# Kernel tuning notes

Measured on AMD Instinct MI355X. Metric: run time of the kernel, lower is better.

## Reference

```python
import jax, jax.numpy as jnp
import numpy as np

N = 100000          # num nodes
E = 1600000         # num edges (before self-loops)
IN = 128            # in_channels
HID = 32            # hidden_channels (= per-head dim, concat=False)
HEADS = 4
NEG_SLOPE = 0.2     # PyG GATConv default


def _glorot(k, shape):
    fan = shape[0] + shape[-1]
    return jax.random.normal(k, shape, jnp.float32) * np.float32(np.sqrt(2.0 / fan))


def setup_inputs() -> dict:
    key = jax.random.key(0)
    ks = jax.random.split(key, 18)
    inp = {}
    inp['x'] = jax.random.normal(ks[0], (N, IN), jnp.float32)
    inp['edge_index'] = jax.random.randint(ks[1], (2, E), 0, N, dtype=jnp.int64)
    dims_in = [IN, HID, HID]
    for i in range(3):
        inp[f'W{i+1}'] = _glorot(ks[2 + 4 * i], (dims_in[i], HEADS * HID))
        inp[f'as{i+1}'] = _glorot(ks[3 + 4 * i], (HEADS, HID))
        inp[f'ad{i+1}'] = _glorot(ks[4 + 4 * i], (HEADS, HID))
        inp[f'b{i+1}'] = jnp.zeros((HID,), jnp.float32)
    inp['lw1'] = _glorot(ks[14], (HID, HID // 2))
    inp['lb1'] = jnp.zeros((HID // 2,), jnp.float32)
    inp['lw2'] = _glorot(ks[15], (HID // 2, 1))
    inp['lb2'] = jnp.zeros((1,), jnp.float32)
    return inp


def gat_conv(x, src, dst, W, a_s, a_d, b):
    # x: [N, F_in]; src/dst: [E'] (self-loops included); concat=False -> head mean
    n = x.shape[0]
    h = (x @ W).reshape(n, HEADS, HID)                      # [N, H, C]
    alpha_src = jnp.einsum('nhc,hc->nh', h, a_s)            # [N, H]
    alpha_dst = jnp.einsum('nhc,hc->nh', h, a_d)            # [N, H]
    e = jax.nn.leaky_relu(alpha_src[src] + alpha_dst[dst], NEG_SLOPE)  # [E', H]
    # softmax over edges grouped by destination node
    e_max = jax.ops.segment_max(e, dst, num_segments=n)     # [N, H]
    e = jnp.exp(e - e_max[dst])
    denom = jax.ops.segment_sum(e, dst, num_segments=n)     # [N, H]
    alpha = e / (denom[dst] + 1e-16)                        # [E', H]
    msg = h[src] * alpha[:, :, None]                        # [E', H, C]
    out = jax.ops.segment_sum(msg, dst, num_segments=n)     # [N, H, C]
    return out.mean(axis=1) + b                             # concat=False: mean heads


def reference(x, edge_index, W1, as1, ad1, b1, W2, as2, ad2, b2, W3, as3, ad3, b3, lw1, lb1, lw2, lb2):
    # add self-loops (PyG GATConv default add_self_loops=True)
    loop = jnp.arange(N, dtype=edge_index.dtype)
    src = jnp.concatenate([edge_index[0], loop])
    dst = jnp.concatenate([edge_index[1], loop])
    h = jax.nn.relu(gat_conv(x, src, dst, W1, as1, ad1, b1))
    h = jax.nn.relu(gat_conv(h, src, dst, W2, as2, ad2, b2))
    h = jax.nn.relu(gat_conv(h, src, dst, W3, as3, ad3, b3))
    g = h.mean(axis=0, keepdims=True)                       # global_mean_pool, batch=None -> [1, HID]
    g = jax.nn.relu(g @ lw1 + lb1)                          # dropout is identity in eval
    return g @ lw2 + lb2                                    # [1, 1]
```

## Files before the change

### kernel.cpp

```cpp
#include <hip/hip_runtime.h>
#include <hip/hip_bf16.h>


#define HEADS 4
#define HID 32
#define F_HID 128
#define NEG_SLOPE 0.2f
#define BSHIFT 5
#define MAXB 3328

typedef float v2f __attribute__((ext_vector_type(2)));
using s8bf  = __attribute__((ext_vector_type(8))) short;
using f32x4 = __attribute__((ext_vector_type(4))) float;

__device__ __forceinline__ float lrelu(float v) { return v > 0.f ? v : NEG_SLOPE * v; }

__device__ __forceinline__ uint32_t bf16_rne(float f) {
    union { float f; uint32_t u; } c; c.f = f;
    return (c.u + 0x7fffu + ((c.u >> 16) & 1u)) >> 16;
}
__device__ __forceinline__ v2f up2(uint32_t u) {
    v2f r;
    r.x = __uint_as_float(u << 16);
    r.y = __uint_as_float(u & 0xffff0000u);
    return r;
}
__device__ __forceinline__ float bperm_f(int addr, float v) {
    return __int_as_float(__builtin_amdgcn_ds_bpermute(addr, __float_as_int(v)));
}
__device__ __forceinline__ int bperm_i(int addr, int v) {
    return __builtin_amdgcn_ds_bpermute(addr, v);
}
__device__ __forceinline__ v2f vshflxor(v2f v, int m) {
    v2f r; r.x = __shfl_xor(v.x, m); r.y = __shfl_xor(v.y, m); return r;
}


__global__ void deg_hist(const int* __restrict__ ei, int E, int* __restrict__ deg) {
    int i = blockIdx.x * blockDim.x + threadIdx.x;
    if (i < E) {
        int d = ei[E + i];
        atomicAdd(&deg[d], 1);
    }
}

__global__ void scan_partial(const int* __restrict__ deg, int n, int* __restrict__ partial) {
    __shared__ int sm[256];
    int t = threadIdx.x;
    int i = blockIdx.x * 256 + t;
    sm[t] = (i < n) ? deg[i] : 0;
    __syncthreads();
    for (int s = 128; s > 0; s >>= 1) {
        if (t < s) sm[t] += sm[t + s];
        __syncthreads();
    }
    if (t == 0) partial[blockIdx.x] = sm[0];
}

__global__ __launch_bounds__(512) void scan_exclusive(int* partial, int B) {
    __shared__ int sm[512];
    int t = threadIdx.x;
    int carry = 0;
    for (int base = 0; base < B; base += 512) {
        int v = (base + t < B) ? partial[base + t] : 0;
        sm[t] = v;
        __syncthreads();
        for (int s = 1; s < 512; s <<= 1) {
            int add = (t >= s) ? sm[t - s] : 0;
            __syncthreads();
            sm[t] += add;
            __syncthreads();
        }
        if (base + t < B) partial[base + t] = carry + sm[t] - v;
        carry += sm[511];
        __syncthreads();
    }
}

__global__ void scan_final(const int* __restrict__ deg, int n, const int* __restrict__ partial,
                           int* __restrict__ row_start, int* __restrict__ gcursor) {
    __shared__ int sm[256];
    int t = threadIdx.x;
    int i = blockIdx.x * 256 + t;
    int v = (i < n) ? deg[i] : 0;
    sm[t] = v;
    __syncthreads();
    for (int s = 1; s < 256; s <<= 1) {
        int add = (t >= s) ? sm[t - s] : 0;
        __syncthreads();
        sm[t] += add;
        __syncthreads();
    }
    if (i < n) {
        int excl = partial[blockIdx.x] + sm[t] - v;
        row_start[i] = excl;
        if ((i & 31) == 0) gcursor[i >> BSHIFT] = excl;
    }
}

__global__ __launch_bounds__(512) void bucket_scatter(const int* __restrict__ ei, int E, int nb,
                                                      int* __restrict__ gcursor,
                                                      uint32_t* __restrict__ tmp) {
    __shared__ int hist[MAXB];
    __shared__ int base[MAXB];
    int t = threadIdx.x;
    int per = (E + gridDim.x - 1) / gridDim.x;
    int e0 = blockIdx.x * per;
    int e1 = e0 + per; if (e1 > E) e1 = E;

    for (int i = t; i < nb; i += 512) hist[i] = 0;
    __syncthreads();
    for (int i = e0 + t; i < e1; i += 512) {
        int d = ei[E + i];
        atomicAdd(&hist[d >> BSHIFT], 1);
    }
    __syncthreads();
    for (int i = t; i < nb; i += 512) {
        int c = hist[i];
        base[i] = c ? atomicAdd(&gcursor[i], c) : 0;
        hist[i] = 0;
    }
    __syncthreads();
    for (int i = e0 + t; i < e1; i += 512) {
        int d = ei[E + i];
        int s = ei[i];
        int b = d >> BSHIFT;
        int loc = atomicAdd(&hist[b], 1);
        tmp[base[b] + loc] = ((uint32_t)s << BSHIFT) | (uint32_t)(d & 31);
    }
}

__global__ __launch_bounds__(256) void bucket_sort(const uint32_t* __restrict__ tmp,
                                                   const int* __restrict__ row_start,
                                                   int n, int E,
                                                   int* __restrict__ csr) {
    __shared__ int cur[32];
    int b = blockIdx.x;
    int node0 = b << BSHIFT;
    int base = row_start[node0];
    int node1 = node0 + 32;
    int end = (node1 < n) ? row_start[node1] : E;
    int cnt = end - base;
    int t = threadIdx.x;
    if (t < 32) {
        int nd = node0 + t;
        cur[t] = (nd < n) ? (row_start[nd] - base) : 0;
    }
    __syncthreads();
    for (int i = t; i < cnt; i += 256) {
        uint32_t v = tmp[base + i];
        int pos = atomicAdd(&cur[v & 31], 1);
        csr[base + pos] = (int)(v >> BSHIFT);
    }
}


template <int FIN>
__global__ void prep_w(const float* __restrict__ W, const float* __restrict__ a_s,
                       const float* __restrict__ a_d, unsigned short* __restrict__ wbt) {
    constexpr int LDK = FIN + 8;
    int t = blockIdx.x * 256 + threadIdx.x;
    if (t >= 144 * LDK) return;
    int r = t / LDK, k = t % LDK;
    float v = 0.f;
    if (k < FIN) {
        if (r < 128) {
            v = W[(size_t)k * F_HID + r];
        } else if (r < 136) {
            int j = r - 128;
            const float* av = (j < 4) ? a_s : a_d;
            int hd = j & 3;
            float s = 0.f;
            for (int c = 0; c < 32; c++)
                s += W[(size_t)k * F_HID + hd * 32 + c] * av[hd * 32 + c];
            v = s;
        }
    }
    wbt[t] = (unsigned short)bf16_rne(v);
}

template <int FIN>
__global__ __launch_bounds__(256) void gemm_mfma(const float* __restrict__ x,
                                                 const unsigned short* __restrict__ wbt,
                                                 uint32_t* __restrict__ hb,
                                                 float* __restrict__ asrc,
                                                 float* __restrict__ adst, int n) {
    constexpr int LDK = FIN + 8;
    __shared__ unsigned short wl[144 * LDK];
    __shared__ unsigned short xs[32 * LDK];
    int t = threadIdx.x;
    int base = blockIdx.x * 32;

    {
        const uint4* wg4 = (const uint4*)wbt;
        uint4* wl4 = (uint4*)wl;
        constexpr int W4 = 144 * LDK / 8;
        for (int i = t; i < W4; i += 256) wl4[i] = wg4[i];
    }
    {
        constexpr int XIT = 32 * FIN / 4;
        for (int idx = t; idx < XIT; idx += 256) {
            int node = idx / (FIN / 4);
            int k4 = (idx % (FIN / 4)) * 4;
            int gnode = base + node;
            float4 v;
            if (gnode < n) v = *(const float4*)&x[(size_t)gnode * FIN + k4];
            else { v.x = 0.f; v.y = 0.f; v.z = 0.f; v.w = 0.f; }
            unsigned short* dst = &xs[node * LDK + k4];
            dst[0] = (unsigned short)bf16_rne(v.x);
            dst[1] = (unsigned short)bf16_rne(v.y);
            dst[2] = (unsigned short)bf16_rne(v.z);
            dst[3] = (unsigned short)bf16_rne(v.w);
        }
    }
    __syncthreads();

    int w = t >> 6;
    int l = t & 63;
    int nt = w >> 1;
    int ct0 = (w & 1) ? 5 : 0;
    int ct1 = (w & 1) ? 9 : 5;
    int lr = l & 15, lg = l >> 4;
    int node = base + nt * 16 + lr;
    const unsigned short* xrow = &xs[(nt * 16 + lr) * LDK + lg * 8];

    for (int ct = ct0; ct < ct1; ct++) {
        f32x4 acc = {0.f, 0.f, 0.f, 0.f};
        const unsigned short* arow = &wl[(ct * 16 + lr) * LDK + lg * 8];
#pragma unroll
        for (int kt = 0; kt < FIN / 32; kt++) {
            s8bf a = *(const s8bf*)(arow + kt * 32);
            s8bf b = *(const s8bf*)(xrow + kt * 32);
            acc = __builtin_amdgcn_mfma_f32_16x16x32_bf16(a, b, acc, 0, 0, 0);
        }
        if (node < n) {
            if (ct < 8) {
                uint2 pp;
                pp.x = bf16_rne(acc[0]) | (bf16_rne(acc[1]) << 16);
                pp.y = bf16_rne(acc[2]) | (bf16_rne(acc[3]) << 16);
                *(uint2*)&hb[(size_t)node * 64 + ct * 8 + lg * 2] = pp;
            } else {
                float4 o; o.x = acc[0]; o.y = acc[1]; o.z = acc[2]; o.w = acc[3];
                if (lg == 0)      *(float4*)&asrc[node * 4] = o;
                else if (lg == 1) *(float4*)&adst[node * 4] = o;
            }
        }
    }
}

__global__ __launch_bounds__(256) void aggregate(const uint32_t* __restrict__ hb,
                                                 const float* __restrict__ asrc,
                                                 const float* __restrict__ adst,
                                                 const int* __restrict__ row_start,
                                                 const int* __restrict__ deg,
                                                 const int* __restrict__ csr_src,
                                                 const float* __restrict__ bias,
                                                 float* __restrict__ xout, int n) {
    int d = blockIdx.x * 4 + (threadIdx.x >> 6);
    if (d >= n) return;
    int l = threadIdx.x & 63;
    int hd = l >> 4;
    int ci = l & 15;
    int hh = (l & 15) >> 2;
    int permH = hh << 6;
    int permb = permH + (l >> 4) * 4;
    int rowoff = hh * 64 + (l & 3) * 16;

    int start = row_start[d];
    int cnt = deg[d];
    float ad = adst[d * HEADS + hd];
    float e_self = lrelu(asrc[d * HEADS + hd] + ad);
    const char* hbbase = (const char*)hb;

    uint4 us = *(const uint4*)(hbbase + (((uint32_t)d) << 8) + rowoff);

    float dsum = 0.f;
    v2f a0 = {0.f, 0.f}, a1 = {0.f, 0.f}, a2 = {0.f, 0.f}, a3 = {0.f, 0.f};
    const int* csr = csr_src + start;

#define ACC4(U, PJ)                         \
    {                                       \
        v2f p2 = {PJ, PJ};                  \
        a0 += p2 * up2((U).x);              \
        a1 += p2 * up2((U).y);              \
        a2 += p2 * up2((U).z);              \
        a3 += p2 * up2((U).w);              \
    }

    for (int j0 = 0; j0 < cnt; j0 += 32) {
        int ncnt = cnt - j0; if (ncnt > 32) ncnt = 32;
        int jA = j0 + ci;      if (jA > cnt - 1) jA = cnt - 1;
        int jB = j0 + 16 + ci; if (jB > cnt - 1) jB = cnt - 1;
        int s0 = csr[jA];
        int s1 = csr[jB];

        int sj0 = bperm_i(permb,      s0);
        int sj1 = bperm_i(permb + 16, s0);
        int sj2 = bperm_i(permb + 32, s0);
        int sj3 = bperm_i(permb + 48, s0);
        int sj4 = bperm_i(permb,      s1);
        int sj5 = bperm_i(permb + 16, s1);
        int sj6 = bperm_i(permb + 32, s1);
        int sj7 = bperm_i(permb + 48, s1);
        uint4 u0 = *(const uint4*)(hbbase + (((uint32_t)sj0) << 8) + rowoff);
        uint4 u1 = *(const uint4*)(hbbase + (((uint32_t)sj1) << 8) + rowoff);
        uint4 u2 = *(const uint4*)(hbbase + (((uint32_t)sj2) << 8) + rowoff);
        uint4 u3 = *(const uint4*)(hbbase + (((uint32_t)sj3) << 8) + rowoff);
        uint4 u4 = *(const uint4*)(hbbase + (((uint32_t)sj4) << 8) + rowoff);
        uint4 u5 = *(const uint4*)(hbbase + (((uint32_t)sj5) << 8) + rowoff);
        uint4 u6 = *(const uint4*)(hbbase + (((uint32_t)sj6) << 8) + rowoff);
        uint4 u7 = *(const uint4*)(hbbase + (((uint32_t)sj7) << 8) + rowoff);

        float pe0 = (ci < ncnt)      ? __expf(lrelu(asrc[s0 * HEADS + hd] + ad)) : 0.f;
        float pe1 = (ci + 16 < ncnt) ? __expf(lrelu(asrc[s1 * HEADS + hd] + ad)) : 0.f;
        dsum += pe0 + pe1;
        float pj0 = bperm_f(permb,      pe0);
        float pj1 = bperm_f(permb + 16, pe0);
        float pj2 = bperm_f(permb + 32, pe0);
        float pj3 = bperm_f(permb + 48, pe0);
        float pj4 = bperm_f(permb,      pe1);
        float pj5 = bperm_f(permb + 16, pe1);
        float pj6 = bperm_f(permb + 32, pe1);
        float pj7 = bperm_f(permb + 48, pe1);

        ACC4(u0, pj0); ACC4(u1, pj1); ACC4(u2, pj2); ACC4(u3, pj3);
        ACC4(u4, pj4); ACC4(u5, pj5); ACC4(u6, pj6); ACC4(u7, pj7);
    }
#undef ACC4

    dsum += __shfl_xor(dsum, 8);
    dsum += __shfl_xor(dsum, 4);
    dsum += __shfl_xor(dsum, 2);
    dsum += __shfl_xor(dsum, 1);
    float ps = __expf(e_self);
    float inv = 1.f / (dsum + ps + 1e-16f);
    float psg = bperm_f(permH, ps);
    float invg = bperm_f(permH, inv);

    a0 += vshflxor(a0, 16); a0 += vshflxor(a0, 32);
    a1 += vshflxor(a1, 16); a1 += vshflxor(a1, 32);
    a2 += vshflxor(a2, 16); a2 += vshflxor(a2, 32);
    a3 += vshflxor(a3, 16); a3 += vshflxor(a3, 32);

    v2f ps2 = {psg, psg};
    a0 += ps2 * up2(us.x);
    a1 += ps2 * up2(us.y);
    a2 += ps2 * up2(us.z);
    a3 += ps2 * up2(us.w);
    v2f iv2 = {invg, invg};
    a0 *= iv2; a1 *= iv2; a2 *= iv2; a3 *= iv2;

    a0 += vshflxor(a0, 4); a0 += vshflxor(a0, 8);
    a1 += vshflxor(a1, 4); a1 += vshflxor(a1, 8);
    a2 += vshflxor(a2, 4); a2 += vshflxor(a2, 8);
    a3 += vshflxor(a3, 4); a3 += vshflxor(a3, 8);

    if (l < 4) {
        const float4* bv = (const float4*)&bias[l * 8];
        float4 b0 = bv[0], b1 = bv[1];
        float4 o0, o1;
        o0.x = 0.25f * a0.x + b0.x; o0.y = 0.25f * a0.y + b0.y;
        o0.z = 0.25f * a1.x + b0.z; o0.w = 0.25f * a1.y + b0.w;
        o1.x = 0.25f * a2.x + b1.x; o1.y = 0.25f * a2.y + b1.y;
        o1.z = 0.25f * a3.x + b1.z; o1.w = 0.25f * a3.y + b1.w;
        o0.x = o0.x > 0.f ? o0.x : 0.f;  o0.y = o0.y > 0.f ? o0.y : 0.f;
        o0.z = o0.z > 0.f ? o0.z : 0.f;  o0.w = o0.w > 0.f ? o0.w : 0.f;
        o1.x = o1.x > 0.f ? o1.x : 0.f;  o1.y = o1.y > 0.f ? o1.y : 0.f;
        o1.z = o1.z > 0.f ? o1.z : 0.f;  o1.w = o1.w > 0.f ? o1.w : 0.f;
        float4* op = (float4*)&xout[(size_t)d * HID + l * 8];
        op[0] = o0;
        op[1] = o1;
    }
}


__global__ void pool_sum(const float* __restrict__ x, int n, float* __restrict__ g) {
    __shared__ float sm[256];
    int t = threadIdx.x;
    int c = t & 31;
    int r = t >> 5;
    float acc = 0.f;
    for (int i = blockIdx.x * 8 + r; i < n; i += gridDim.x * 8)
        acc += x[(size_t)i * HID + c];
    sm[t] = acc;
    __syncthreads();
    if (t < 32) {
        float v = 0.f;
#pragma unroll
        for (int k = 0; k < 8; k++) v += sm[t + 32 * k];
        atomicAdd(&g[t], v);
    }
}

__global__ void mlp_final(const float* __restrict__ g,
                          const float* __restrict__ lw1, const float* __restrict__ lb1,
                          const float* __restrict__ lw2, const float* __restrict__ lb2,
                          float* __restrict__ out, float invn) {
    __shared__ float gm[32];
    int t = threadIdx.x;
    if (t < 32) gm[t] = g[t] * invn;
    __syncthreads();
    float q = 0.f;
    if (t < 16) {
        q = lb1[t];
        for (int c = 0; c < 32; c++) q += gm[c] * lw1[c * 16 + t];
        q = q > 0.f ? q : 0.f;
        q *= lw2[t];
    }
#pragma unroll
    for (int off = 8; off >= 1; off >>= 1) q += __shfl_xor(q, off);
    if (t == 0) out[0] = q + lb2[0];
}


extern "C" void kernel_launch(void* const* d_in, const int* in_sizes, int n_in,
                              void* d_out, int out_size, void* d_ws, size_t ws_size,
                              hipStream_t stream) {
    const float* x   = (const float*)d_in[0];
    const int*   ei  = (const int*)d_in[1];
    const float* W1  = (const float*)d_in[2];
    const float* as1 = (const float*)d_in[3];
    const float* ad1 = (const float*)d_in[4];
    const float* b1  = (const float*)d_in[5];
    const float* W2  = (const float*)d_in[6];
    const float* as2 = (const float*)d_in[7];
    const float* ad2 = (const float*)d_in[8];
    const float* b2  = (const float*)d_in[9];
    const float* W3  = (const float*)d_in[10];
    const float* as3 = (const float*)d_in[11];
    const float* ad3 = (const float*)d_in[12];
    const float* b3  = (const float*)d_in[13];
    const float* lw1 = (const float*)d_in[14];
    const float* lb1 = (const float*)d_in[15];
    const float* lw2 = (const float*)d_in[16];
    const float* lb2 = (const float*)d_in[17];
    float* out = (float*)d_out;

    int n = in_sizes[0] / 128;
    int E = in_sizes[1] / 2;
    int B = (n + 255) / 256;
    int nb = (n + 31) >> BSHIFT;

    char* p = (char*)d_ws;
    auto alloc = [&](size_t bytes) -> void* {
        void* r = (void*)p;
        p += (bytes + 255) & ~(size_t)255;
        return r;
    };
    int* deg       = (int*)alloc((size_t)n * 4);
    int* row_start = (int*)alloc((size_t)n * 4);
    int* gcursor   = (int*)alloc((size_t)nb * 4);
    int* partial   = (int*)alloc((size_t)B * 4);
    int* csr       = (int*)alloc((size_t)E * 4);
    uint32_t* tmp  = (uint32_t*)alloc((size_t)E * 4);
    float* asrc    = (float*)alloc((size_t)n * HEADS * 4);
    float* adst    = (float*)alloc((size_t)n * HEADS * 4);
    uint32_t* hb   = (uint32_t*)alloc((size_t)n * 64 * 4);
    float* xA      = (float*)alloc((size_t)n * HID * 4);
    float* xB      = (float*)alloc((size_t)n * HID * 4);
    float* g       = (float*)alloc(32 * 4);
    unsigned short* wbt = (unsigned short*)alloc((size_t)144 * 136 * 2);

    hipMemsetAsync(deg, 0, (size_t)n * 4, stream);
    deg_hist<<<(E + 255) / 256, 256, 0, stream>>>(ei, E, deg);
    scan_partial<<<B, 256, 0, stream>>>(deg, n, partial);
    scan_exclusive<<<1, 512, 0, stream>>>(partial, B);
    scan_final<<<B, 256, 0, stream>>>(deg, n, partial, row_start, gcursor);
    bucket_scatter<<<64, 512, 0, stream>>>(ei, E, nb, gcursor, tmp);
    bucket_sort<<<nb, 256, 0, stream>>>(tmp, row_start, n, E, csr);

    int gb = (n + 31) / 32;
    int ggb = (n + 3) / 4;
    int wg128 = (144 * 136 + 255) / 256;
    int wg32  = (144 * 40 + 255) / 256;

    prep_w<128><<<wg128, 256, 0, stream>>>(W1, as1, ad1, wbt);
    gemm_mfma<128><<<gb, 256, 0, stream>>>(x, wbt, hb, asrc, adst, n);
    aggregate<<<ggb, 256, 0, stream>>>(hb, asrc, adst, row_start, deg, csr, b1, xA, n);

    prep_w<32><<<wg32, 256, 0, stream>>>(W2, as2, ad2, wbt);
    gemm_mfma<32><<<gb, 256, 0, stream>>>(xA, wbt, hb, asrc, adst, n);
    aggregate<<<ggb, 256, 0, stream>>>(hb, asrc, adst, row_start, deg, csr, b2, xB, n);

    prep_w<32><<<wg32, 256, 0, stream>>>(W3, as3, ad3, wbt);
    gemm_mfma<32><<<gb, 256, 0, stream>>>(xB, wbt, hb, asrc, adst, n);
    aggregate<<<ggb, 256, 0, stream>>>(hb, asrc, adst, row_start, deg, csr, b3, xA, n);

    hipMemsetAsync(g, 0, 32 * 4, stream);
    pool_sum<<<256, 256, 0, stream>>>(xA, n, g);
    mlp_final<<<1, 64, 0, stream>>>(g, lw1, lb1, lw2, lb2, out, 1.0f / (float)n);
}
```

Baseline: 464.7 us.

## Build CSR from bucket histogram and enlarge GEMM node tile to 64

Replaces the per-node degree histogram with global atomics and the three-kernel scan by a shared-memory bucket histogram and a single scan over 32-node buckets. Per-node degrees and row starts are now derived inside bucket_sort through a local count and prefix. This removes the global-atomic histogram pass and two scan kernels. The GEMM now handles 64 nodes per block, with each wave computing all 9 column tiles for its own 16 rows, so each block's LDS weight load serves more nodes. The bucket scatter grid also grows from 64 to 256 blocks. In exchange, bucket_sort reads its bucket twice and uses a serial 32-entry prefix.

Result: faster. 403.8 us (-13.1%).

```diff
diff --git a/kernel.cpp b/kernel.cpp
--- a/kernel.cpp
+++ b/kernel.cpp
@@ -36,33 +36,30 @@
 }
 
 
-__global__ void deg_hist(const int* __restrict__ ei, int E, int* __restrict__ deg) {
-    int i = blockIdx.x * blockDim.x + threadIdx.x;
-    if (i < E) {
-        int d = ei[E + i];
-        atomicAdd(&deg[d], 1);
-    }
-}
-
-__global__ void scan_partial(const int* __restrict__ deg, int n, int* __restrict__ partial) {
-    __shared__ int sm[256];
-    int t = threadIdx.x;
-    int i = blockIdx.x * 256 + t;
-    sm[t] = (i < n) ? deg[i] : 0;
-    __syncthreads();
-    for (int s = 128; s > 0; s >>= 1) {
-        if (t < s) sm[t] += sm[t + s];
-        __syncthreads();
-    }
-    if (t == 0) partial[blockIdx.x] = sm[0];
-}
-
-__global__ __launch_bounds__(512) void scan_exclusive(int* partial, int B) {
+__global__ __launch_bounds__(256) void bucket_hist(const int* __restrict__ ei, int E, int nb,
+                                                   int* __restrict__ bcnt) {
+    __shared__ int h[MAXB];
+    int t = threadIdx.x;
+    for (int i = t; i < nb; i += 256) h[i] = 0;
+    __syncthreads();
+    int per = (E + gridDim.x - 1) / gridDim.x;
+    int e0 = blockIdx.x * per;
+    int e1 = e0 + per; if (e1 > E) e1 = E;
+    for (int i = e0 + t; i < e1; i += 256)
+        atomicAdd(&h[ei[E + i] >> BSHIFT], 1);
+    __syncthreads();
+    for (int i = t; i < nb; i += 256)
+        if (h[i]) atomicAdd(&bcnt[i], h[i]);
+}
+
+__global__ __launch_bounds__(512) void bucket_scan(const int* __restrict__ bcnt, int nb,
+                                                   int* __restrict__ gbase,
+                                                   int* __restrict__ gcursor) {
     __shared__ int sm[512];
     int t = threadIdx.x;
     int carry = 0;
-    for (int base = 0; base < B; base += 512) {
-        int v = (base + t < B) ? partial[base + t] : 0;
+    for (int b0 = 0; b0 < nb; b0 += 512) {
+        int v = (b0 + t < nb) ? bcnt[b0 + t] : 0;
         sm[t] = v;
         __syncthreads();
         for (int s = 1; s < 512; s <<= 1) {
@@ -71,31 +68,15 @@
             sm[t] += add;
             __syncthreads();
         }
-        if (base + t < B) partial[base + t] = carry + sm[t] - v;
+        if (b0 + t < nb) {
+            int ex = carry + sm[t] - v;
+            gbase[b0 + t] = ex;
+            gcursor[b0 + t] = ex;
+        }
         carry += sm[511];
         __syncthreads();
     }
-}
-
-__global__ void scan_final(const int* __restrict__ deg, int n, const int* __restrict__ partial,
-                           int* __restrict__ row_start, int* __restrict__ gcursor) {
-    __shared__ int sm[256];
-    int t = threadIdx.x;
-    int i = blockIdx.x * 256 + t;
-    int v = (i < n) ? deg[i] : 0;
-    sm[t] = v;
-    __syncthreads();
-    for (int s = 1; s < 256; s <<= 1) {
-        int add = (t >= s) ? sm[t - s] : 0;
-        __syncthreads();
-        sm[t] += add;
-        __syncthreads();
-    }
-    if (i < n) {
-        int excl = partial[blockIdx.x] + sm[t] - v;
-        row_start[i] = excl;
-        if ((i & 31) == 0) gcursor[i >> BSHIFT] = excl;
-    }
+    if (t == 0) gbase[nb] = carry;
 }
 
 __global__ __launch_bounds__(512) void bucket_scatter(const int* __restrict__ ei, int E, int nb,
@@ -131,25 +112,38 @@
 }
 
 __global__ __launch_bounds__(256) void bucket_sort(const uint32_t* __restrict__ tmp,
-                                                   const int* __restrict__ row_start,
-                                                   int n, int E,
-                                                   int* __restrict__ csr) {
-    __shared__ int cur[32];
+                                                   const int* __restrict__ gbase,
+                                                   int n, int* __restrict__ csr,
+                                                   int* __restrict__ row_start,
+                                                   int* __restrict__ deg) {
+    __shared__ int cnt[32], pre[32];
     int b = blockIdx.x;
     int node0 = b << BSHIFT;
-    int base = row_start[node0];
-    int node1 = node0 + 32;
-    int end = (node1 < n) ? row_start[node1] : E;
-    int cnt = end - base;
-    int t = threadIdx.x;
+    int base = gbase[b];
+    int cntE = gbase[b + 1] - base;
+    int t = threadIdx.x;
+    if (t < 32) cnt[t] = 0;
+    __syncthreads();
+    for (int i = t; i < cntE; i += 256)
+        atomicAdd(&cnt[tmp[base + i] & 31], 1);
+    __syncthreads();
+    if (t == 0) {
+        int run = 0;
+        for (int i = 0; i < 32; i++) { pre[i] = run; run += cnt[i]; }
+    }
+    __syncthreads();
     if (t < 32) {
         int nd = node0 + t;
-        cur[t] = (nd < n) ? (row_start[nd] - base) : 0;
-    }
-    __syncthreads();
-    for (int i = t; i < cnt; i += 256) {
+        if (nd < n) {
+            row_start[nd] = base + pre[t];
+            deg[nd] = cnt[t];
+        }
+        cnt[t] = pre[t];
+    }
+    __syncthreads();
+    for (int i = t; i < cntE; i += 256) {
         uint32_t v = tmp[base + i];
-        int pos = atomicAdd(&cur[v & 31], 1);
+        int pos = atomicAdd(&cnt[v & 31], 1);
         csr[base + pos] = (int)(v >> BSHIFT);
     }
 }
@@ -186,10 +180,11 @@
                                                  float* __restrict__ asrc,
                                                  float* __restrict__ adst, int n) {
     constexpr int LDK = FIN + 8;
+    constexpr int NPB = 64;
     __shared__ unsigned short wl[144 * LDK];
-    __shared__ unsigned short xs[32 * LDK];
-    int t = threadIdx.x;
-    int base = blockIdx.x * 32;
+    __shared__ unsigned short xs[NPB * LDK];
+    int t = threadIdx.x;
+    int base = blockIdx.x * NPB;
 
     {
         const uint4* wg4 = (const uint4*)wbt;
@@ -198,7 +193,7 @@
         for (int i = t; i < W4; i += 256) wl4[i] = wg4[i];
     }
     {
-        constexpr int XIT = 32 * FIN / 4;
+        constexpr int XIT = NPB * FIN / 4;
         for (int idx = t; idx < XIT; idx += 256) {
             int node = idx / (FIN / 4);
             int k4 = (idx % (FIN / 4)) * 4;
@@ -217,14 +212,11 @@
 
     int w = t >> 6;
     int l = t & 63;
-    int nt = w >> 1;
-    int ct0 = (w & 1) ? 5 : 0;
-    int ct1 = (w & 1) ? 9 : 5;
     int lr = l & 15, lg = l >> 4;
-    int node = base + nt * 16 + lr;
-    const unsigned short* xrow = &xs[(nt * 16 + lr) * LDK + lg * 8];
-
-    for (int ct = ct0; ct < ct1; ct++) {
+    int node = base + w * 16 + lr;
+    const unsigned short* xrow = &xs[(w * 16 + lr) * LDK + lg * 8];
+
+    for (int ct = 0; ct < 9; ct++) {
         f32x4 acc = {0.f, 0.f, 0.f, 0.f};
         const unsigned short* arow = &wl[(ct * 16 + lr) * LDK + lg * 8];
 #pragma unroll
@@ -438,7 +430,6 @@
 
     int n = in_sizes[0] / 128;
     int E = in_sizes[1] / 2;
-    int B = (n + 255) / 256;
     int nb = (n + 31) >> BSHIFT;
 
     char* p = (char*)d_ws;
@@ -449,8 +440,9 @@
     };
     int* deg       = (int*)alloc((size_t)n * 4);
     int* row_start = (int*)alloc((size_t)n * 4);
+    int* bcnt      = (int*)alloc((size_t)nb * 4);
+    int* gbase     = (int*)alloc((size_t)(nb + 1) * 4);
     int* gcursor   = (int*)alloc((size_t)nb * 4);
-    int* partial   = (int*)alloc((size_t)B * 4);
     int* csr       = (int*)alloc((size_t)E * 4);
     uint32_t* tmp  = (uint32_t*)alloc((size_t)E * 4);
     float* asrc    = (float*)alloc((size_t)n * HEADS * 4);
@@ -461,15 +453,13 @@
     float* g       = (float*)alloc(32 * 4);
     unsigned short* wbt = (unsigned short*)alloc((size_t)144 * 136 * 2);
 
-    hipMemsetAsync(deg, 0, (size_t)n * 4, stream);
-    deg_hist<<<(E + 255) / 256, 256, 0, stream>>>(ei, E, deg);
-    scan_partial<<<B, 256, 0, stream>>>(deg, n, partial);
-    scan_exclusive<<<1, 512, 0, stream>>>(partial, B);
-    scan_final<<<B, 256, 0, stream>>>(deg, n, partial, row_start, gcursor);
-    bucket_scatter<<<64, 512, 0, stream>>>(ei, E, nb, gcursor, tmp);
-    bucket_sort<<<nb, 256, 0, stream>>>(tmp, row_start, n, E, csr);
-
-    int gb = (n + 31) / 32;
+    hipMemsetAsync(bcnt, 0, (size_t)nb * 4, stream);
+    bucket_hist<<<256, 256, 0, stream>>>(ei, E, nb, bcnt);
+    bucket_scan<<<1, 512, 0, stream>>>(bcnt, nb, gbase, gcursor);
+    bucket_scatter<<<256, 512, 0, stream>>>(ei, E, nb, gcursor, tmp);
+    bucket_sort<<<nb, 256, 0, stream>>>(tmp, gbase, n, csr, row_start, deg);
+
+    int gb = (n + 63) / 64;
     int ggb = (n + 3) / 4;
     int wg128 = (144 * 136 + 255) / 256;
     int wg32  = (144 * 40 + 255) / 256;
```
